# Kernel tuning notes

Measured on AMD Instinct MI355X. Metric: run time of the kernel, lower is better.

Reference implementation:

```python
import jax, jax.numpy as jnp
import numpy as np

N, E, H, IN_FEAT, NUM_GRAPHS, NUM_CLASSES, L, HID = 50000, 600000, 128, 7, 256, 2, 5, 256
EPS_MSG = 1e-7
EPS_SOFTMAX = 1e-16
LN_EPS = 1e-5


def layer_norm(x, g, b):
    mu = jnp.mean(x, axis=-1, keepdims=True)
    var = jnp.mean((x - mu) ** 2, axis=-1, keepdims=True)
    return (x - mu) * jax.lax.rsqrt(var + LN_EPS) * g + b


def setup_inputs() -> dict:
    key = jax.random.key(0)
    ks = jax.random.split(key, 16)
    s = 0.05
    return {
        "x": jax.random.normal(ks[0], (N, IN_FEAT), jnp.float32),
        "edge_index": jax.random.randint(ks[1], (2, E), 0, N),
        "batch": jnp.sort(jax.random.randint(ks[2], (N,), 0, NUM_GRAPHS)),
        "enc_W": jax.random.normal(ks[3], (IN_FEAT, H), jnp.float32) * s,
        "enc_b": jnp.zeros((H,), jnp.float32),
        "t": jnp.ones((L,), jnp.float32),  # learn_t, init t=1.0
        "W1": jax.random.normal(ks[4], (L, H, HID), jnp.float32) * s,
        "b1": jnp.zeros((L, HID), jnp.float32),
        "g1": jnp.ones((L, HID), jnp.float32),
        "bb1": jnp.zeros((L, HID), jnp.float32),
        "W2": jax.random.normal(ks[5], (L, HID, H), jnp.float32) * s,
        "b2": jnp.zeros((L, H), jnp.float32),
        "ln_g": jnp.ones((L, H), jnp.float32),
        "ln_b": jnp.zeros((L, H), jnp.float32),
        "cls_W": jax.random.normal(ks[6], (H, NUM_CLASSES), jnp.float32) * s,
        "cls_b": jnp.zeros((NUM_CLASSES,), jnp.float32),
    }


def reference(x, edge_index, batch, enc_W, enc_b, t, W1, b1, g1, bb1, W2, b2, ln_g, ln_b, cls_W, cls_b):
    n = x.shape[0]
    src, dst = edge_index[0], edge_index[1]  # messages flow src -> dst
    h = x @ enc_W + enc_b  # node_encoder, [N, H]
    for i in range(t.shape[0]):  # DeepGCNLayer, block='res+'
        z = jax.nn.relu(layer_norm(h, ln_g[i], ln_b[i]))
        # GENConv message: relu(x_j) + eps (edge_attr is None)
        msg = jax.nn.relu(z[src]) + EPS_MSG  # [E, H]
        # scatter-softmax aggregation with temperature t
        logits = msg * t[i]
        m = jax.ops.segment_max(logits, dst, num_segments=n)  # [N, H]
        ex = jnp.exp(logits - m[dst])
        den = jax.ops.segment_sum(ex, dst, num_segments=n) + EPS_SOFTMAX
        agg = jax.ops.segment_sum(ex * msg, dst, num_segments=n) / den
        # GENConv update MLP: Linear -> LayerNorm -> ReLU -> Linear on (agg + x)
        out = agg + z
        hm = jax.nn.relu(layer_norm(out @ W1[i] + b1[i], g1[i], bb1[i]))
        h = h + (hm @ W2[i] + b2[i])  # residual
    pooled = jax.ops.segment_sum(h, batch, num_segments=NUM_GRAPHS)  # global_add_pool
    return pooled @ cls_W + cls_b
```

## Files before the change

kernel.cpp:

```cpp
#include <hip/hip_runtime.h>
#include <hip/hip_bf16.h>

#define HD 128
#define HIDD 256
#define EPS_MSG 1e-7f
#define EPS_SM 1e-16f
#define LN_EPS 1e-5f
#define HP2 264
#define LOG2E 1.44269504f

typedef __attribute__((ext_vector_type(8))) short bf16x8;
typedef __attribute__((ext_vector_type(4))) float f32x4;
typedef __attribute__((ext_vector_type(4))) ushort u16x4;

static __device__ __forceinline__ float wave_reduce_sum(float v) {
#pragma unroll
    for (int off = 32; off >= 1; off >>= 1) v += __shfl_xor(v, off, 64);
    return v;
}

static __device__ __forceinline__ float u2f(unsigned v) {
    union { float f; unsigned u; } x;
    x.u = v;
    return x.f;
}
static __device__ __forceinline__ ushort f2bf(float f) {
    __hip_bfloat16 b = __float2bfloat16(f);
    return *(ushort*)&b;
}
static __device__ __forceinline__ unsigned packbf(float lo, float hi) {
    return (unsigned)f2bf(lo) | ((unsigned)f2bf(hi) << 16);
}

__global__ __launch_bounds__(256) void enc_ln_kernel(const float* __restrict__ x,
                                                     const float* __restrict__ W,
                                                     const float* __restrict__ b,
                                                     const float* __restrict__ g,
                                                     const float* __restrict__ bt,
                                                     unsigned* __restrict__ hp,
                                                     unsigned* __restrict__ zp, int N) {
    int node = blockIdx.x * 4 + (threadIdx.x >> 6);
    int lane = threadIdx.x & 63;
    if (node >= N) return;
    float xr[7];
#pragma unroll
    for (int j = 0; j < 7; ++j) xr[j] = x[node * 7 + j];
    float v0 = b[lane], v1 = b[lane + 64];
#pragma unroll
    for (int j = 0; j < 7; ++j) {
        v0 = fmaf(xr[j], W[j * HD + lane], v0);
        v1 = fmaf(xr[j], W[j * HD + lane + 64], v1);
    }
    float s = wave_reduce_sum(v0 + v1);
    float ss = wave_reduce_sum(v0 * v0 + v1 * v1);
    float mu = s * (1.f / 128.f);
    float var = ss * (1.f / 128.f) - mu * mu;
    float rstd = rsqrtf(var + LN_EPS);
    float z0 = fmaxf((v0 - mu) * rstd * g[lane] + bt[lane], 0.f);
    float z1 = fmaxf((v1 - mu) * rstd * g[lane + 64] + bt[lane + 64], 0.f);
    int i0 = (2 * lane) & 63, i1 = (2 * lane + 1) & 63;
    float he_lo = __shfl(v0, i0), ho_lo = __shfl(v0, i1);
    float he_hi = __shfl(v1, i0), ho_hi = __shfl(v1, i1);
    float hce = (lane < 32) ? he_lo : he_hi;
    float hco = (lane < 32) ? ho_lo : ho_hi;
    hp[(size_t)node * 64 + lane] = packbf(hce, hco);
    float e_lo = __shfl(z0, i0), o_lo = __shfl(z0, i1);
    float e_hi = __shfl(z1, i0), o_hi = __shfl(z1, i1);
    float ce = (lane < 32) ? e_lo : e_hi;
    float co = (lane < 32) ? o_lo : o_hi;
    zp[(size_t)node * 64 + lane] = packbf(ce, co);
}

__global__ __launch_bounds__(256) void wconv_kernel(const float* __restrict__ W1,
                                                    const float* __restrict__ W2,
                                                    ushort* __restrict__ W1t,
                                                    ushort* __restrict__ W2t, int L) {
    int gid = blockIdx.x * 256 + threadIdx.x;
    int per = HD * HIDD;
    int tot = L * per;
    if (gid < tot) {
        int l = gid / per, r = gid % per;
        int n = r >> 7, k = r & 127;
        W1t[gid] = f2bf(W1[(size_t)l * per + (size_t)k * HIDD + n]);
    } else if (gid < 2 * tot) {
        int g2 = gid - tot;
        int l = g2 / per, r = g2 % per;
        int n = r >> 8, k = r & 255;
        W2t[g2] = f2bf(W2[(size_t)l * per + (size_t)k * HD + n]);
    }
}

__global__ __launch_bounds__(256) void count_kernel(const int* __restrict__ dst, int* __restrict__ cnt, int E) {
    int e = blockIdx.x * 256 + threadIdx.x;
    if (e < E) atomicAdd(&cnt[dst[e]], 1);
}

__global__ __launch_bounds__(256) void scanA_kernel(const int* __restrict__ cnt, int* __restrict__ row_ptr,
                                                    int* __restrict__ blk_sums, int n) {
    __shared__ int sb[256];
    int tid = threadIdx.x;
    int idx = blockIdx.x * 256 + tid;
    int v = (idx < n) ? cnt[idx] : 0;
    sb[tid] = v;
    __syncthreads();
#pragma unroll
    for (int off = 1; off < 256; off <<= 1) {
        int x = (tid >= off) ? sb[tid - off] : 0;
        __syncthreads();
        sb[tid] += x;
        __syncthreads();
    }
    if (idx < n) row_ptr[idx + 1] = sb[tid];
    if (tid == 255) blk_sums[blockIdx.x] = sb[255];
}

__global__ __launch_bounds__(256) void scanB_kernel(int* __restrict__ blk_sums, int nblk) {
    __shared__ int sb[256];
    int tid = threadIdx.x;
    int v = (tid < nblk) ? blk_sums[tid] : 0;
    sb[tid] = v;
    __syncthreads();
#pragma unroll
    for (int off = 1; off < 256; off <<= 1) {
        int x = (tid >= off) ? sb[tid - off] : 0;
        __syncthreads();
        sb[tid] += x;
        __syncthreads();
    }
    if (tid < nblk) blk_sums[tid] = sb[tid];
}

__global__ __launch_bounds__(256) void scanC_kernel(int* __restrict__ row_ptr, const int* __restrict__ blk_sums, int n) {
    int idx = blockIdx.x * 256 + threadIdx.x;
    if (idx == 0) row_ptr[0] = 0;
    if (idx < n) {
        int b = idx >> 8;
        if (b > 0) row_ptr[idx + 1] += blk_sums[b - 1];
    }
}

__global__ __launch_bounds__(256) void cursor_init_kernel(const int* __restrict__ row_ptr, int* __restrict__ cursor, int n) {
    int idx = blockIdx.x * 256 + threadIdx.x;
    if (idx < n) cursor[idx] = row_ptr[idx];
}

__global__ __launch_bounds__(256) void scatter_kernel(const int* __restrict__ src, const int* __restrict__ dst,
                                                      int* __restrict__ cursor, int* __restrict__ esrc, int E) {
    int e = blockIdx.x * 256 + threadIdx.x;
    if (e < E) {
        int v = dst[e];
        int pos = atomicAdd(&cursor[v], 1);
        esrc[pos] = src[e];
    }
}

__global__ __launch_bounds__(256) void agg_kernel(const unsigned* __restrict__ zp,
                                                  const int* __restrict__ row_ptr,
                                                  const int* __restrict__ esrc,
                                                  const float* __restrict__ t_all, int layer,
                                                  unsigned* __restrict__ obuf, int N) {
    int node = __builtin_amdgcn_readfirstlane(blockIdx.x * 4 + (threadIdx.x >> 6));
    int lane = threadIdx.x & 63;
    if (node >= N) return;
    const float tv = t_all[layer];
    const float M = 12.f * fmaxf(tv, 1.f);
    const float tv2 = tv * LOG2E;
    const float mM2 = -M * LOG2E;
    int beg = row_ptr[node], end = row_ptr[node + 1];

    float se0 = 0.f, se1 = 0.f, sw0 = 0.f, sw1 = 0.f;
    float te0 = 0.f, te1 = 0.f, tw0 = 0.f, tw1 = 0.f;

#define AGG_EDGE(P, E0, E1, W0, W1)                                   \
    {                                                                  \
        float a0 = u2f((P) << 16) + EPS_MSG;                           \
        float a1 = u2f((P) & 0xffff0000u) + EPS_MSG;                   \
        float x0 = __builtin_amdgcn_exp2f(fmaf(a0, tv2, mM2));         \
        float x1 = __builtin_amdgcn_exp2f(fmaf(a1, tv2, mM2));         \
        E0 += x0;                                                      \
        E1 += x1;                                                      \
        W0 = fmaf(x0, a0, W0);                                         \
        W1 = fmaf(x1, a1, W1);                                         \
    }

    int e = beg;
    for (; e + 4 <= end; e += 4) {
        int s0 = esrc[e], s1 = esrc[e + 1], s2 = esrc[e + 2], s3 = esrc[e + 3];
        unsigned p0 = zp[(size_t)s0 * 64 + lane];
        unsigned p1 = zp[(size_t)s1 * 64 + lane];
        unsigned p2 = zp[(size_t)s2 * 64 + lane];
        unsigned p3 = zp[(size_t)s3 * 64 + lane];
        AGG_EDGE(p0, se0, se1, sw0, sw1)
        AGG_EDGE(p1, se0, se1, sw0, sw1)
        AGG_EDGE(p2, te0, te1, tw0, tw1)
        AGG_EDGE(p3, te0, te1, tw0, tw1)
    }
    for (; e < end; ++e) {
        unsigned p0 = zp[(size_t)esrc[e] * 64 + lane];
        AGG_EDGE(p0, se0, se1, sw0, sw1)
    }
#undef AGG_EDGE
    se0 += te0; se1 += te1; sw0 += tw0; sw1 += tw1;

    float a0 = (end > beg) ? sw0 / (se0 + EPS_SM) : 0.f;
    float a1 = (end > beg) ? sw1 / (se1 + EPS_SM) : 0.f;
    unsigned ps = zp[(size_t)node * 64 + lane];
    float z0 = u2f(ps << 16), z1 = u2f(ps & 0xffff0000u);
    obuf[(size_t)node * 64 + lane] = packbf(a0 + z0, a1 + z1);
}

__global__ __launch_bounds__(256, 4) void mlp_kernel(const ushort* __restrict__ obuf,
                                                     unsigned* __restrict__ hp,
                                                     const ushort* __restrict__ W1t, const float* __restrict__ b1,
                                                     const float* __restrict__ g1, const float* __restrict__ bb1,
                                                     const ushort* __restrict__ W2t, const float* __restrict__ b2,
                                                     const float* __restrict__ gnext, const float* __restrict__ btnext,
                                                     unsigned* __restrict__ zp, int fuse,
                                                     int N) {
    __shared__ ushort s_hm[32 * HP2];
    __shared__ float s_part[32 * 8];

    int tid = threadIdx.x;
    int wid = tid >> 6, lane = tid & 63;
    int l15 = lane & 15, q = lane >> 4;
    int row0 = blockIdx.x * 32;

    uint2 hpre[2][2];
#pragma unroll
    for (int mb = 0; mb < 2; ++mb) {
        int row = row0 + mb * 16 + l15;
#pragma unroll
        for (int nb = 0; nb < 2; ++nb) {
            if (row < N)
                hpre[mb][nb] = *(const uint2*)&hp[(size_t)row * 64 + wid * 16 + nb * 8 + q * 2];
            else {
                hpre[mb][nb].x = 0u;
                hpre[mb][nb].y = 0u;
            }
        }
    }

    f32x4 acc1[2][4];
#pragma unroll
    for (int mb = 0; mb < 2; ++mb)
#pragma unroll
        for (int nb = 0; nb < 4; ++nb) acc1[mb][nb] = (f32x4)0.f;

#pragma unroll
    for (int kk = 0; kk < 4; ++kk) {
        bf16x8 bfr[2];
#pragma unroll
        for (int mb = 0; mb < 2; ++mb) {
            int row = row0 + mb * 16 + l15;
            if (row < N)
                bfr[mb] = *(const bf16x8*)(obuf + (size_t)row * HD + kk * 32 + q * 8);
            else
                bfr[mb] = (bf16x8)0;
        }
#pragma unroll
        for (int nb = 0; nb < 4; ++nb) {
            bf16x8 wfr = *(const bf16x8*)&W1t[(size_t)(wid * 64 + nb * 16 + l15) * HD + kk * 32 + q * 8];
#pragma unroll
            for (int mb = 0; mb < 2; ++mb)
                acc1[mb][nb] = __builtin_amdgcn_mfma_f32_16x16x32_bf16(wfr, bfr[mb], acc1[mb][nb], 0, 0, 0);
        }
    }

    f32x4 b1v[4];
#pragma unroll
    for (int nb = 0; nb < 4; ++nb) b1v[nb] = *(const f32x4*)&b1[wid * 64 + nb * 16 + q * 4];

#pragma unroll
    for (int mb = 0; mb < 2; ++mb) {
        float s = 0.f, ss = 0.f;
#pragma unroll
        for (int nb = 0; nb < 4; ++nb) {
#pragma unroll
            for (int rg = 0; rg < 4; ++rg) {
                float v = acc1[mb][nb][rg] + b1v[nb][rg];
                acc1[mb][nb][rg] = v;
                s += v;
                ss += v * v;
            }
        }
        s += __shfl_xor(s, 16, 64);
        s += __shfl_xor(s, 32, 64);
        ss += __shfl_xor(ss, 16, 64);
        ss += __shfl_xor(ss, 32, 64);
        if (q == 0) {
            s_part[(mb * 16 + l15) * 8 + wid * 2] = s;
            s_part[(mb * 16 + l15) * 8 + wid * 2 + 1] = ss;
        }
    }
    __syncthreads();

    f32x4 g1v[4], bbv[4];
#pragma unroll
    for (int nb = 0; nb < 4; ++nb) {
        g1v[nb] = *(const f32x4*)&g1[wid * 64 + nb * 16 + q * 4];
        bbv[nb] = *(const f32x4*)&bb1[wid * 64 + nb * 16 + q * 4];
    }
#pragma unroll
    for (int mb = 0; mb < 2; ++mb) {
        int rl = mb * 16 + l15;
        f32x4 p0 = *(const f32x4*)&s_part[rl * 8];
        f32x4 p1 = *(const f32x4*)&s_part[rl * 8 + 4];
        float S = p0.x + p0.z + p1.x + p1.z;
        float SS = p0.y + p0.w + p1.y + p1.w;
        float mu = S * (1.f / 256.f);
        float var = SS * (1.f / 256.f) - mu * mu;
        float rstd = rsqrtf(var + LN_EPS);
#pragma unroll
        for (int nb = 0; nb < 4; ++nb) {
            u16x4 pk;
#pragma unroll
            for (int rg = 0; rg < 4; ++rg) {
                float v = fmaxf((acc1[mb][nb][rg] - mu) * rstd * g1v[nb][rg] + bbv[nb][rg], 0.f);
                pk[rg] = f2bf(v);
            }
            *(u16x4*)&s_hm[rl * HP2 + wid * 64 + nb * 16 + q * 4] = pk;
        }
    }
    __syncthreads();

    f32x4 acc2[2][2];
#pragma unroll
    for (int mb = 0; mb < 2; ++mb)
#pragma unroll
        for (int nb = 0; nb < 2; ++nb) acc2[mb][nb] = (f32x4)0.f;

#pragma unroll
    for (int kk = 0; kk < 8; ++kk) {
        bf16x8 hfr[2];
#pragma unroll
        for (int mb = 0; mb < 2; ++mb)
            hfr[mb] = *(const bf16x8*)&s_hm[(mb * 16 + l15) * HP2 + kk * 32 + q * 8];
#pragma unroll
        for (int nb = 0; nb < 2; ++nb) {
            bf16x8 wfr = *(const bf16x8*)&W2t[(size_t)(wid * 32 + nb * 16 + l15) * HIDD + kk * 32 + q * 8];
#pragma unroll
            for (int mb = 0; mb < 2; ++mb)
                acc2[mb][nb] = __builtin_amdgcn_mfma_f32_16x16x32_bf16(wfr, hfr[mb], acc2[mb][nb], 0, 0, 0);
        }
    }

    f32x4 b2v[2];
#pragma unroll
    for (int nb = 0; nb < 2; ++nb) b2v[nb] = *(const f32x4*)&b2[wid * 32 + nb * 16 + q * 4];

#pragma unroll
    for (int mb = 0; mb < 2; ++mb) {
        int row = row0 + mb * 16 + l15;
        float s2 = 0.f, ss2 = 0.f;
        if (row < N) {
#pragma unroll
            for (int nb = 0; nb < 2; ++nb) {
                uint2 hv = hpre[mb][nb];
                float h0 = u2f(hv.x << 16), h1 = u2f(hv.x & 0xffff0000u);
                float h2 = u2f(hv.y << 16), h3 = u2f(hv.y & 0xffff0000u);
                f32x4 v;
                v[0] = h0 + acc2[mb][nb][0] + b2v[nb][0];
                v[1] = h1 + acc2[mb][nb][1] + b2v[nb][1];
                v[2] = h2 + acc2[mb][nb][2] + b2v[nb][2];
                v[3] = h3 + acc2[mb][nb][3] + b2v[nb][3];
                s2 += v[0] + v[1] + v[2] + v[3];
                ss2 += v[0] * v[0] + v[1] * v[1] + v[2] * v[2] + v[3] * v[3];
                uint2 pk;
                pk.x = packbf(v[0], v[1]);
                pk.y = packbf(v[2], v[3]);
                *(uint2*)&hp[(size_t)row * 64 + wid * 16 + nb * 8 + q * 2] = pk;
                acc2[mb][nb] = v;
            }
        }
        if (fuse) {
            s2 += __shfl_xor(s2, 16, 64);
            s2 += __shfl_xor(s2, 32, 64);
            ss2 += __shfl_xor(ss2, 16, 64);
            ss2 += __shfl_xor(ss2, 32, 64);
            if (q == 0) {
                s_part[(mb * 16 + l15) * 8 + wid * 2] = s2;
                s_part[(mb * 16 + l15) * 8 + wid * 2 + 1] = ss2;
            }
        }
    }

    if (fuse) {
        __syncthreads();
        f32x4 gnv[2], bnv[2];
#pragma unroll
        for (int nb = 0; nb < 2; ++nb) {
            gnv[nb] = *(const f32x4*)&gnext[wid * 32 + nb * 16 + q * 4];
            bnv[nb] = *(const f32x4*)&btnext[wid * 32 + nb * 16 + q * 4];
        }
#pragma unroll
        for (int mb = 0; mb < 2; ++mb) {
            int rl = mb * 16 + l15;
            int row = row0 + rl;
            f32x4 p0 = *(const f32x4*)&s_part[rl * 8];
            f32x4 p1 = *(const f32x4*)&s_part[rl * 8 + 4];
            float S = p0.x + p0.z + p1.x + p1.z;
            float SS = p0.y + p0.w + p1.y + p1.w;
            float mu = S * (1.f / 128.f);
            float var = SS * (1.f / 128.f) - mu * mu;
            float rstd = rsqrtf(var + LN_EPS);
            if (row < N) {
#pragma unroll
                for (int nb = 0; nb < 2; ++nb) {
                    float z0 = fmaxf((acc2[mb][nb][0] - mu) * rstd * gnv[nb][0] + bnv[nb][0], 0.f);
                    float z1 = fmaxf((acc2[mb][nb][1] - mu) * rstd * gnv[nb][1] + bnv[nb][1], 0.f);
                    float z2 = fmaxf((acc2[mb][nb][2] - mu) * rstd * gnv[nb][2] + bnv[nb][2], 0.f);
                    float z3 = fmaxf((acc2[mb][nb][3] - mu) * rstd * gnv[nb][3] + bnv[nb][3], 0.f);
                    uint2 pk;
                    pk.x = packbf(z0, z1);
                    pk.y = packbf(z2, z3);
                    *(uint2*)&zp[(size_t)row * 64 + wid * 16 + nb * 8 + q * 2] = pk;
                }
            }
        }
    }
}

__global__ __launch_bounds__(256) void pool_kernel(const unsigned* __restrict__ hp,
                                                   const int* __restrict__ batch, int N,
                                                   float* __restrict__ pooled) {
    __shared__ int sb[2];
    __shared__ float red0[256], red1[256];
    int g = blockIdx.x;
    if (threadIdx.x == 0) {
        int lo = 0, hi = N;
        while (lo < hi) { int mid = (lo + hi) >> 1; if (batch[mid] < g) lo = mid + 1; else hi = mid; }
        sb[0] = lo;
        lo = 0; hi = N;
        int gq = g + 1;
        while (lo < hi) { int mid = (lo + hi) >> 1; if (batch[mid] < gq) lo = mid + 1; else hi = mid; }
        sb[1] = lo;
    }
    __syncthreads();
    int beg = sb[0], end = sb[1];
    int c = threadIdx.x & 63, str = threadIdx.x >> 6;
    float a0 = 0.f, a1 = 0.f;
    for (int r = beg + str; r < end; r += 4) {
        unsigned p = hp[(size_t)r * 64 + c];
        a0 += u2f(p << 16);
        a1 += u2f(p & 0xffff0000u);
    }
    red0[threadIdx.x] = a0;
    red1[threadIdx.x] = a1;
    __syncthreads();
    if (str == 0) {
        float s0 = red0[c] + red0[64 + c] + red0[128 + c] + red0[192 + c];
        float s1 = red1[c] + red1[64 + c] + red1[128 + c] + red1[192 + c];
        pooled[(size_t)g * HD + 2 * c] = s0;
        pooled[(size_t)g * HD + 2 * c + 1] = s1;
    }
}

__global__ __launch_bounds__(256) void cls_kernel(const float* __restrict__ pooled,
                                                  const float* __restrict__ W,
                                                  const float* __restrict__ b,
                                                  float* __restrict__ out, int G) {
    int gid = blockIdx.x * 256 + threadIdx.x;
    if (gid >= G * 2) return;
    int g = gid >> 1, cl = gid & 1;
    float acc = b[cl];
#pragma unroll 8
    for (int k = 0; k < HD; ++k) acc += pooled[g * HD + k] * W[k * 2 + cl];
    out[gid] = acc;
}

extern "C" void kernel_launch(void* const* d_in, const int* in_sizes, int n_in,
                              void* d_out, int out_size, void* d_ws, size_t ws_size,
                              hipStream_t stream) {
    const float* x     = (const float*)d_in[0];
    const int*   eidx  = (const int*)d_in[1];
    const int*   batch = (const int*)d_in[2];
    const float* enc_W = (const float*)d_in[3];
    const float* enc_b = (const float*)d_in[4];
    const float* t_all = (const float*)d_in[5];
    const float* W1    = (const float*)d_in[6];
    const float* b1    = (const float*)d_in[7];
    const float* g1    = (const float*)d_in[8];
    const float* bb1   = (const float*)d_in[9];
    const float* W2    = (const float*)d_in[10];
    const float* b2    = (const float*)d_in[11];
    const float* ln_g  = (const float*)d_in[12];
    const float* ln_b  = (const float*)d_in[13];
    const float* cls_W = (const float*)d_in[14];
    const float* cls_b = (const float*)d_in[15];
    float* out = (float*)d_out;

    const int N = in_sizes[0] / 7;
    const int E = in_sizes[1] / 2;
    const int L = in_sizes[5];
    const int G = out_size / 2;
    const int* src = eidx;
    const int* dst = eidx + E;

    char* p = (char*)d_ws;
    auto alloc = [&](size_t bytes) {
        char* q = p;
        p += (bytes + 255) & ~(size_t)255;
        return q;
    };
    unsigned* hp     = (unsigned*)alloc((size_t)N * 64 * 4);
    unsigned* zp     = (unsigned*)alloc((size_t)N * 64 * 4);
    unsigned* obuf   = (unsigned*)alloc((size_t)N * 64 * 4);
    float*    pooled = (float*)alloc((size_t)G * HD * 4);
    int* cnt      = (int*)alloc((size_t)N * 4);
    int* row_ptr  = (int*)alloc((size_t)(N + 1) * 4);
    int* cursor   = (int*)alloc((size_t)N * 4);
    int* blk_sums = (int*)alloc(256 * 4);
    int* esrc     = (int*)alloc((size_t)E * 4);
    ushort* W1t   = (ushort*)alloc((size_t)L * HD * HIDD * 2);
    ushort* W2t   = (ushort*)alloc((size_t)L * HD * HIDD * 2);

    const int nblkN = (N + 255) / 256;
    const int nblkE = (E + 255) / 256;

    enc_ln_kernel<<<(N + 3) / 4, 256, 0, stream>>>(x, enc_W, enc_b, ln_g, ln_b, hp, zp, N);
    {
        int tot2 = 2 * L * HD * HIDD;
        wconv_kernel<<<(tot2 + 255) / 256, 256, 0, stream>>>(W1, W2, W1t, W2t, L);
    }

    hipMemsetAsync(cnt, 0, (size_t)N * 4, stream);
    count_kernel<<<nblkE, 256, 0, stream>>>(dst, cnt, E);
    scanA_kernel<<<nblkN, 256, 0, stream>>>(cnt, row_ptr, blk_sums, N);
    scanB_kernel<<<1, 256, 0, stream>>>(blk_sums, nblkN);
    scanC_kernel<<<nblkN, 256, 0, stream>>>(row_ptr, blk_sums, N);
    cursor_init_kernel<<<nblkN, 256, 0, stream>>>(row_ptr, cursor, N);
    scatter_kernel<<<nblkE, 256, 0, stream>>>(src, dst, cursor, esrc, E);

    for (int i = 0; i < L; ++i) {
        agg_kernel<<<(N + 3) / 4, 256, 0, stream>>>(zp, row_ptr, esrc, t_all, i, obuf, N);
        int fuse = (i + 1 < L) ? 1 : 0;
        const float* gn = ln_g + (size_t)(fuse ? i + 1 : i) * HD;
        const float* bn = ln_b + (size_t)(fuse ? i + 1 : i) * HD;
        mlp_kernel<<<(N + 31) / 32, 256, 0, stream>>>((const ushort*)obuf, hp,
                                                      W1t + (size_t)i * HD * HIDD, b1 + (size_t)i * HIDD,
                                                      g1 + (size_t)i * HIDD, bb1 + (size_t)i * HIDD,
                                                      W2t + (size_t)i * HD * HIDD, b2 + (size_t)i * HD,
                                                      gn, bn, zp, fuse, N);
    }

    pool_kernel<<<G, 256, 0, stream>>>(hp, batch, N, pooled);
    cls_kernel<<<(G * 2 + 255) / 256, 256, 0, stream>>>(pooled, cls_W, cls_b, out, G);
}
```

Baseline: 495.2 us.

## Persistent MLP kernel with register-resident weights, prefetching agg loop, fused cursor init

The MLP kernel becomes persistent with a 512-block grid. Each wave loads its W1 and W2 MFMA fragments into registers once and loops over 32-row tiles, so weights are not re-read per tile; it adds a sync at the top of each tile to protect shared-memory reuse. The aggregation kernel now software-pipelines its gathers, loading the next four source rows before processing the current ones, and issues the self-row load early. The cursor-init kernel is merged into scanC, which removes one launch. Holding the weights in registers raises register pressure (launch bounds occupancy hint dropped), which may cut occupancy.

```diff
diff --git a/kernel.cpp b/kernel.cpp
--- a/kernel.cpp
+++ b/kernel.cpp
@@ -130,18 +130,16 @@
     if (tid < nblk) blk_sums[tid] = sb[tid];
 }
 
-__global__ __launch_bounds__(256) void scanC_kernel(int* __restrict__ row_ptr, const int* __restrict__ blk_sums, int n) {
+__global__ __launch_bounds__(256) void scanC_kernel(int* __restrict__ row_ptr, const int* __restrict__ blk_sums,
+                                                    int* __restrict__ cursor, int n) {
     int idx = blockIdx.x * 256 + threadIdx.x;
-    if (idx == 0) row_ptr[0] = 0;
+    if (idx == 0) { row_ptr[0] = 0; cursor[0] = 0; }
     if (idx < n) {
         int b = idx >> 8;
-        if (b > 0) row_ptr[idx + 1] += blk_sums[b - 1];
-    }
-}
-
-__global__ __launch_bounds__(256) void cursor_init_kernel(const int* __restrict__ row_ptr, int* __restrict__ cursor, int n) {
-    int idx = blockIdx.x * 256 + threadIdx.x;
-    if (idx < n) cursor[idx] = row_ptr[idx];
+        int v = row_ptr[idx + 1] + ((b > 0) ? blk_sums[b - 1] : 0);
+        row_ptr[idx + 1] = v;
+        if (idx + 1 < n) cursor[idx + 1] = v;
+    }
 }
 
 __global__ __launch_bounds__(256) void scatter_kernel(const int* __restrict__ src, const int* __restrict__ dst,
@@ -168,6 +166,8 @@
     const float mM2 = -M * LOG2E;
     int beg = row_ptr[node], end = row_ptr[node + 1];
 
+    unsigned ps = zp[(size_t)node * 64 + lane];
+
     float se0 = 0.f, se1 = 0.f, sw0 = 0.f, sw1 = 0.f;
     float te0 = 0.f, te1 = 0.f, tw0 = 0.f, tw1 = 0.f;
 
@@ -184,16 +184,35 @@
     }
 
     int e = beg;
-    for (; e + 4 <= end; e += 4) {
+    unsigned pc0, pc1, pc2, pc3;
+    int have = 0;
+    if (e + 4 <= end) {
         int s0 = esrc[e], s1 = esrc[e + 1], s2 = esrc[e + 2], s3 = esrc[e + 3];
-        unsigned p0 = zp[(size_t)s0 * 64 + lane];
-        unsigned p1 = zp[(size_t)s1 * 64 + lane];
-        unsigned p2 = zp[(size_t)s2 * 64 + lane];
-        unsigned p3 = zp[(size_t)s3 * 64 + lane];
-        AGG_EDGE(p0, se0, se1, sw0, sw1)
-        AGG_EDGE(p1, se0, se1, sw0, sw1)
-        AGG_EDGE(p2, te0, te1, tw0, tw1)
-        AGG_EDGE(p3, te0, te1, tw0, tw1)
+        pc0 = zp[(size_t)s0 * 64 + lane];
+        pc1 = zp[(size_t)s1 * 64 + lane];
+        pc2 = zp[(size_t)s2 * 64 + lane];
+        pc3 = zp[(size_t)s3 * 64 + lane];
+        have = 4;
+        e += 4;
+    }
+    while (have == 4) {
+        unsigned pn0, pn1, pn2, pn3;
+        int haven = 0;
+        if (e + 4 <= end) {
+            int s0 = esrc[e], s1 = esrc[e + 1], s2 = esrc[e + 2], s3 = esrc[e + 3];
+            pn0 = zp[(size_t)s0 * 64 + lane];
+            pn1 = zp[(size_t)s1 * 64 + lane];
+            pn2 = zp[(size_t)s2 * 64 + lane];
+            pn3 = zp[(size_t)s3 * 64 + lane];
+            haven = 4;
+            e += 4;
+        }
+        AGG_EDGE(pc0, se0, se1, sw0, sw1)
+        AGG_EDGE(pc1, se0, se1, sw0, sw1)
+        AGG_EDGE(pc2, te0, te1, tw0, tw1)
+        AGG_EDGE(pc3, te0, te1, tw0, tw1)
+        pc0 = pn0; pc1 = pn1; pc2 = pn2; pc3 = pn3;
+        have = haven;
     }
     for (; e < end; ++e) {
         unsigned p0 = zp[(size_t)esrc[e] * 64 + lane];
@@ -204,216 +223,220 @@
 
     float a0 = (end > beg) ? sw0 / (se0 + EPS_SM) : 0.f;
     float a1 = (end > beg) ? sw1 / (se1 + EPS_SM) : 0.f;
-    unsigned ps = zp[(size_t)node * 64 + lane];
     float z0 = u2f(ps << 16), z1 = u2f(ps & 0xffff0000u);
     obuf[(size_t)node * 64 + lane] = packbf(a0 + z0, a1 + z1);
 }
 
-__global__ __launch_bounds__(256, 4) void mlp_kernel(const ushort* __restrict__ obuf,
-                                                     unsigned* __restrict__ hp,
-                                                     const ushort* __restrict__ W1t, const float* __restrict__ b1,
-                                                     const float* __restrict__ g1, const float* __restrict__ bb1,
-                                                     const ushort* __restrict__ W2t, const float* __restrict__ b2,
-                                                     const float* __restrict__ gnext, const float* __restrict__ btnext,
-                                                     unsigned* __restrict__ zp, int fuse,
-                                                     int N) {
+__global__ __launch_bounds__(256) void mlp_kernel(const ushort* __restrict__ obuf,
+                                                  unsigned* __restrict__ hp,
+                                                  const ushort* __restrict__ W1t, const float* __restrict__ b1,
+                                                  const float* __restrict__ g1, const float* __restrict__ bb1,
+                                                  const ushort* __restrict__ W2t, const float* __restrict__ b2,
+                                                  const float* __restrict__ gnext, const float* __restrict__ btnext,
+                                                  unsigned* __restrict__ zp, int fuse,
+                                                  int ntiles, int N) {
     __shared__ ushort s_hm[32 * HP2];
     __shared__ float s_part[32 * 8];
 
     int tid = threadIdx.x;
     int wid = tid >> 6, lane = tid & 63;
     int l15 = lane & 15, q = lane >> 4;
-    int row0 = blockIdx.x * 32;
-
-    uint2 hpre[2][2];
-#pragma unroll
-    for (int mb = 0; mb < 2; ++mb) {
-        int row = row0 + mb * 16 + l15;
-#pragma unroll
-        for (int nb = 0; nb < 2; ++nb) {
-            if (row < N)
-                hpre[mb][nb] = *(const uint2*)&hp[(size_t)row * 64 + wid * 16 + nb * 8 + q * 2];
-            else {
-                hpre[mb][nb].x = 0u;
-                hpre[mb][nb].y = 0u;
-            }
-        }
-    }
-
-    f32x4 acc1[2][4];
-#pragma unroll
-    for (int mb = 0; mb < 2; ++mb)
-#pragma unroll
-        for (int nb = 0; nb < 4; ++nb) acc1[mb][nb] = (f32x4)0.f;
-
-#pragma unroll
-    for (int kk = 0; kk < 4; ++kk) {
-        bf16x8 bfr[2];
+
+    bf16x8 w1f[4][4];
+#pragma unroll
+    for (int kk = 0; kk < 4; ++kk)
+#pragma unroll
+        for (int nb = 0; nb < 4; ++nb)
+            w1f[kk][nb] = *(const bf16x8*)&W1t[(size_t)(wid * 64 + nb * 16 + l15) * HD + kk * 32 + q * 8];
+    bf16x8 w2f[8][2];
+#pragma unroll
+    for (int kk = 0; kk < 8; ++kk)
+#pragma unroll
+        for (int nb = 0; nb < 2; ++nb)
+            w2f[kk][nb] = *(const bf16x8*)&W2t[(size_t)(wid * 32 + nb * 16 + l15) * HIDD + kk * 32 + q * 8];
+
+    for (int tile = blockIdx.x; tile < ntiles; tile += gridDim.x) {
+        int row0 = tile * 32;
+
+        uint2 hpre[2][2];
+        bf16x8 bfr[4][2];
 #pragma unroll
         for (int mb = 0; mb < 2; ++mb) {
             int row = row0 + mb * 16 + l15;
-            if (row < N)
-                bfr[mb] = *(const bf16x8*)(obuf + (size_t)row * HD + kk * 32 + q * 8);
-            else
-                bfr[mb] = (bf16x8)0;
-        }
+            if (row < N) {
+#pragma unroll
+                for (int nb = 0; nb < 2; ++nb)
+                    hpre[mb][nb] = *(const uint2*)&hp[(size_t)row * 64 + wid * 16 + nb * 8 + q * 2];
+#pragma unroll
+                for (int kk = 0; kk < 4; ++kk)
+                    bfr[kk][mb] = *(const bf16x8*)(obuf + (size_t)row * HD + kk * 32 + q * 8);
+            } else {
+#pragma unroll
+                for (int nb = 0; nb < 2; ++nb) { hpre[mb][nb].x = 0u; hpre[mb][nb].y = 0u; }
+#pragma unroll
+                for (int kk = 0; kk < 4; ++kk) bfr[kk][mb] = (bf16x8)0;
+            }
+        }
+        __syncthreads();
+
+        f32x4 acc1[2][4];
+#pragma unroll
+        for (int mb = 0; mb < 2; ++mb)
+#pragma unroll
+            for (int nb = 0; nb < 4; ++nb) acc1[mb][nb] = (f32x4)0.f;
+#pragma unroll
+        for (int kk = 0; kk < 4; ++kk)
+#pragma unroll
+            for (int nb = 0; nb < 4; ++nb)
+#pragma unroll
+                for (int mb = 0; mb < 2; ++mb)
+                    acc1[mb][nb] = __builtin_amdgcn_mfma_f32_16x16x32_bf16(w1f[kk][nb], bfr[kk][mb], acc1[mb][nb], 0, 0, 0);
+
+        f32x4 b1v[4];
+#pragma unroll
+        for (int nb = 0; nb < 4; ++nb) b1v[nb] = *(const f32x4*)&b1[wid * 64 + nb * 16 + q * 4];
+#pragma unroll
+        for (int mb = 0; mb < 2; ++mb) {
+            float s = 0.f, ss = 0.f;
+#pragma unroll
+            for (int nb = 0; nb < 4; ++nb) {
+#pragma unroll
+                for (int rg = 0; rg < 4; ++rg) {
+                    float v = acc1[mb][nb][rg] + b1v[nb][rg];
+                    acc1[mb][nb][rg] = v;
+                    s += v;
+                    ss += v * v;
+                }
+            }
+            s += __shfl_xor(s, 16, 64);
+            s += __shfl_xor(s, 32, 64);
+            ss += __shfl_xor(ss, 16, 64);
+            ss += __shfl_xor(ss, 32, 64);
+            if (q == 0) {
+                s_part[(mb * 16 + l15) * 8 + wid * 2] = s;
+                s_part[(mb * 16 + l15) * 8 + wid * 2 + 1] = ss;
+            }
+        }
+        __syncthreads();
+
+        f32x4 g1v[4], bbv[4];
 #pragma unroll
         for (int nb = 0; nb < 4; ++nb) {
-            bf16x8 wfr = *(const bf16x8*)&W1t[(size_t)(wid * 64 + nb * 16 + l15) * HD + kk * 32 + q * 8];
-#pragma unroll
-            for (int mb = 0; mb < 2; ++mb)
-                acc1[mb][nb] = __builtin_amdgcn_mfma_f32_16x16x32_bf16(wfr, bfr[mb], acc1[mb][nb], 0, 0, 0);
-        }
-    }
-
-    f32x4 b1v[4];
-#pragma unroll
-    for (int nb = 0; nb < 4; ++nb) b1v[nb] = *(const f32x4*)&b1[wid * 64 + nb * 16 + q * 4];
-
-#pragma unroll
-    for (int mb = 0; mb < 2; ++mb) {
-        float s = 0.f, ss = 0.f;
-#pragma unroll
-        for (int nb = 0; nb < 4; ++nb) {
-#pragma unroll
-            for (int rg = 0; rg < 4; ++rg) {
-                float v = acc1[mb][nb][rg] + b1v[nb][rg];
-                acc1[mb][nb][rg] = v;
-                s += v;
-                ss += v * v;
-            }
-        }
-        s += __shfl_xor(s, 16, 64);
-        s += __shfl_xor(s, 32, 64);
-        ss += __shfl_xor(ss, 16, 64);
-        ss += __shfl_xor(ss, 32, 64);
-        if (q == 0) {
-            s_part[(mb * 16 + l15) * 8 + wid * 2] = s;
-            s_part[(mb * 16 + l15) * 8 + wid * 2 + 1] = ss;
-        }
-    }
-    __syncthreads();
-
-    f32x4 g1v[4], bbv[4];
-#pragma unroll
-    for (int nb = 0; nb < 4; ++nb) {
-        g1v[nb] = *(const f32x4*)&g1[wid * 64 + nb * 16 + q * 4];
-        bbv[nb] = *(const f32x4*)&bb1[wid * 64 + nb * 16 + q * 4];
-    }
-#pragma unroll
-    for (int mb = 0; mb < 2; ++mb) {
-        int rl = mb * 16 + l15;
-        f32x4 p0 = *(const f32x4*)&s_part[rl * 8];
-        f32x4 p1 = *(const f32x4*)&s_part[rl * 8 + 4];
-        float S = p0.x + p0.z + p1.x + p1.z;
-        float SS = p0.y + p0.w + p1.y + p1.w;
-        float mu = S * (1.f / 256.f);
-        float var = SS * (1.f / 256.f) - mu * mu;
-        float rstd = rsqrtf(var + LN_EPS);
-#pragma unroll
-        for (int nb = 0; nb < 4; ++nb) {
-            u16x4 pk;
-#pragma unroll
-            for (int rg = 0; rg < 4; ++rg) {
-                float v = fmaxf((acc1[mb][nb][rg] - mu) * rstd * g1v[nb][rg] + bbv[nb][rg], 0.f);
-                pk[rg] = f2bf(v);
-            }
-            *(u16x4*)&s_hm[rl * HP2 + wid * 64 + nb * 16 + q * 4] = pk;
-        }
-    }
-    __syncthreads();
-
-    f32x4 acc2[2][2];
-#pragma unroll
-    for (int mb = 0; mb < 2; ++mb)
-#pragma unroll
-        for (int nb = 0; nb < 2; ++nb) acc2[mb][nb] = (f32x4)0.f;
-
-#pragma unroll
-    for (int kk = 0; kk < 8; ++kk) {
-        bf16x8 hfr[2];
-#pragma unroll
-        for (int mb = 0; mb < 2; ++mb)
-            hfr[mb] = *(const bf16x8*)&s_hm[(mb * 16 + l15) * HP2 + kk * 32 + q * 8];
-#pragma unroll
-        for (int nb = 0; nb < 2; ++nb) {
-            bf16x8 wfr = *(const bf16x8*)&W2t[(size_t)(wid * 32 + nb * 16 + l15) * HIDD + kk * 32 + q * 8];
-#pragma unroll
-            for (int mb = 0; mb < 2; ++mb)
-                acc2[mb][nb] = __builtin_amdgcn_mfma_f32_16x16x32_bf16(wfr, hfr[mb], acc2[mb][nb], 0, 0, 0);
-        }
-    }
-
-    f32x4 b2v[2];
-#pragma unroll
-    for (int nb = 0; nb < 2; ++nb) b2v[nb] = *(const f32x4*)&b2[wid * 32 + nb * 16 + q * 4];
-
-#pragma unroll
-    for (int mb = 0; mb < 2; ++mb) {
-        int row = row0 + mb * 16 + l15;
-        float s2 = 0.f, ss2 = 0.f;
-        if (row < N) {
-#pragma unroll
-            for (int nb = 0; nb < 2; ++nb) {
-                uint2 hv = hpre[mb][nb];
-                float h0 = u2f(hv.x << 16), h1 = u2f(hv.x & 0xffff0000u);
-                float h2 = u2f(hv.y << 16), h3 = u2f(hv.y & 0xffff0000u);
-                f32x4 v;
-                v[0] = h0 + acc2[mb][nb][0] + b2v[nb][0];
-                v[1] = h1 + acc2[mb][nb][1] + b2v[nb][1];
-                v[2] = h2 + acc2[mb][nb][2] + b2v[nb][2];
-                v[3] = h3 + acc2[mb][nb][3] + b2v[nb][3];
-                s2 += v[0] + v[1] + v[2] + v[3];
-                ss2 += v[0] * v[0] + v[1] * v[1] + v[2] * v[2] + v[3] * v[3];
-                uint2 pk;
-                pk.x = packbf(v[0], v[1]);
-                pk.y = packbf(v[2], v[3]);
-                *(uint2*)&hp[(size_t)row * 64 + wid * 16 + nb * 8 + q * 2] = pk;
-                acc2[mb][nb] = v;
-            }
-        }
-        if (fuse) {
-            s2 += __shfl_xor(s2, 16, 64);
-            s2 += __shfl_xor(s2, 32, 64);
-            ss2 += __shfl_xor(ss2, 16, 64);
-            ss2 += __shfl_xor(ss2, 32, 64);
-            if (q == 0) {
-                s_part[(mb * 16 + l15) * 8 + wid * 2] = s2;
-                s_part[(mb * 16 + l15) * 8 + wid * 2 + 1] = ss2;
-            }
-        }
-    }
-
-    if (fuse) {
-        __syncthreads();
-        f32x4 gnv[2], bnv[2];
-#pragma unroll
-        for (int nb = 0; nb < 2; ++nb) {
-            gnv[nb] = *(const f32x4*)&gnext[wid * 32 + nb * 16 + q * 4];
-            bnv[nb] = *(const f32x4*)&btnext[wid * 32 + nb * 16 + q * 4];
+            g1v[nb] = *(const f32x4*)&g1[wid * 64 + nb * 16 + q * 4];
+            bbv[nb] = *(const f32x4*)&bb1[wid * 64 + nb * 16 + q * 4];
         }
 #pragma unroll
         for (int mb = 0; mb < 2; ++mb) {
             int rl = mb * 16 + l15;
-            int row = row0 + rl;
             f32x4 p0 = *(const f32x4*)&s_part[rl * 8];
             f32x4 p1 = *(const f32x4*)&s_part[rl * 8 + 4];
             float S = p0.x + p0.z + p1.x + p1.z;
             float SS = p0.y + p0.w + p1.y + p1.w;
-            float mu = S * (1.f / 128.f);
-            float var = SS * (1.f / 128.f) - mu * mu;
+            float mu = S * (1.f / 256.f);
+            float var = SS * (1.f / 256.f) - mu * mu;
             float rstd = rsqrtf(var + LN_EPS);
+#pragma unroll
+            for (int nb = 0; nb < 4; ++nb) {
+                u16x4 pk;
+#pragma unroll
+                for (int rg = 0; rg < 4; ++rg) {
+                    float v = fmaxf((acc1[mb][nb][rg] - mu) * rstd * g1v[nb][rg] + bbv[nb][rg], 0.f);
+                    pk[rg] = f2bf(v);
+                }
+                *(u16x4*)&s_hm[rl * HP2 + wid * 64 + nb * 16 + q * 4] = pk;
+            }
+        }
+        __syncthreads();
+
+        f32x4 acc2[2][2];
+#pragma unroll
+        for (int mb = 0; mb < 2; ++mb)
+#pragma unroll
+            for (int nb = 0; nb < 2; ++nb) acc2[mb][nb] = (f32x4)0.f;
+#pragma unroll
+        for (int kk = 0; kk < 8; ++kk) {
+            bf16x8 hfr[2];
+#pragma unroll
+            for (int mb = 0; mb < 2; ++mb)
+                hfr[mb] = *(const bf16x8*)&s_hm[(mb * 16 + l15) * HP2 + kk * 32 + q * 8];
+#pragma unroll
+            for (int nb = 0; nb < 2; ++nb)
+#pragma unroll
+                for (int mb = 0; mb < 2; ++mb)
+                    acc2[mb][nb] = __builtin_amdgcn_mfma_f32_16x16x32_bf16(w2f[kk][nb], hfr[mb], acc2[mb][nb], 0, 0, 0);
+        }
+
+        f32x4 b2v[2];
+#pragma unroll
+        for (int nb = 0; nb < 2; ++nb) b2v[nb] = *(const f32x4*)&b2[wid * 32 + nb * 16 + q * 4];
+
+#pragma unroll
+        for (int mb = 0; mb < 2; ++mb) {
+            int row = row0 + mb * 16 + l15;
+            float s2 = 0.f, ss2 = 0.f;
             if (row < N) {
 #pragma unroll
                 for (int nb = 0; nb < 2; ++nb) {
-                    float z0 = fmaxf((acc2[mb][nb][0] - mu) * rstd * gnv[nb][0] + bnv[nb][0], 0.f);
-                    float z1 = fmaxf((acc2[mb][nb][1] - mu) * rstd * gnv[nb][1] + bnv[nb][1], 0.f);
-                    float z2 = fmaxf((acc2[mb][nb][2] - mu) * rstd * gnv[nb][2] + bnv[nb][2], 0.f);
-                    float z3 = fmaxf((acc2[mb][nb][3] - mu) * rstd * gnv[nb][3] + bnv[nb][3], 0.f);
+                    uint2 hv = hpre[mb][nb];
+                    float h0 = u2f(hv.x << 16), h1 = u2f(hv.x & 0xffff0000u);
+                    float h2 = u2f(hv.y << 16), h3 = u2f(hv.y & 0xffff0000u);
+                    f32x4 v;
+                    v[0] = h0 + acc2[mb][nb][0] + b2v[nb][0];
+                    v[1] = h1 + acc2[mb][nb][1] + b2v[nb][1];
+                    v[2] = h2 + acc2[mb][nb][2] + b2v[nb][2];
+                    v[3] = h3 + acc2[mb][nb][3] + b2v[nb][3];
+                    s2 += v[0] + v[1] + v[2] + v[3];
+                    ss2 += v[0] * v[0] + v[1] * v[1] + v[2] * v[2] + v[3] * v[3];
                     uint2 pk;
-                    pk.x = packbf(z0, z1);
-                    pk.y = packbf(z2, z3);
-                    *(uint2*)&zp[(size_t)row * 64 + wid * 16 + nb * 8 + q * 2] = pk;
+                    pk.x = packbf(v[0], v[1]);
+                    pk.y = packbf(v[2], v[3]);
+                    *(uint2*)&hp[(size_t)row * 64 + wid * 16 + nb * 8 + q * 2] = pk;
+                    acc2[mb][nb] = v;
+                }
+            }
+            if (fuse) {
+                s2 += __shfl_xor(s2, 16, 64);
+                s2 += __shfl_xor(s2, 32, 64);
+                ss2 += __shfl_xor(ss2, 16, 64);
+                ss2 += __shfl_xor(ss2, 32, 64);
+                if (q == 0) {
+                    s_part[(mb * 16 + l15) * 8 + wid * 2] = s2;
+                    s_part[(mb * 16 + l15) * 8 + wid * 2 + 1] = ss2;
+                }
+            }
+        }
+
+        if (fuse) {
+            __syncthreads();
+            f32x4 gnv[2], bnv[2];
+#pragma unroll
+            for (int nb = 0; nb < 2; ++nb) {
+                gnv[nb] = *(const f32x4*)&gnext[wid * 32 + nb * 16 + q * 4];
+                bnv[nb] = *(const f32x4*)&btnext[wid * 32 + nb * 16 + q * 4];
+            }
+#pragma unroll
+            for (int mb = 0; mb < 2; ++mb) {
+                int rl = mb * 16 + l15;
+                int row = row0 + rl;
+                f32x4 p0 = *(const f32x4*)&s_part[rl * 8];
+                f32x4 p1 = *(const f32x4*)&s_part[rl * 8 + 4];
+                float S = p0.x + p0.z + p1.x + p1.z;
+                float SS = p0.y + p0.w + p1.y + p1.w;
+                float mu = S * (1.f / 128.f);
+                float var = SS * (1.f / 128.f) - mu * mu;
+                float rstd = rsqrtf(var + LN_EPS);
+                if (row < N) {
+#pragma unroll
+                    for (int nb = 0; nb < 2; ++nb) {
+                        float z0 = fmaxf((acc2[mb][nb][0] - mu) * rstd * gnv[nb][0] + bnv[nb][0], 0.f);
+                        float z1 = fmaxf((acc2[mb][nb][1] - mu) * rstd * gnv[nb][1] + bnv[nb][1], 0.f);
+                        float z2 = fmaxf((acc2[mb][nb][2] - mu) * rstd * gnv[nb][2] + bnv[nb][2], 0.f);
+                        float z3 = fmaxf((acc2[mb][nb][3] - mu) * rstd * gnv[nb][3] + bnv[nb][3], 0.f);
+                        uint2 pk;
+                        pk.x = packbf(z0, z1);
+                        pk.y = packbf(z2, z3);
+                        *(uint2*)&zp[(size_t)row * 64 + wid * 16 + nb * 8 + q * 2] = pk;
+                    }
                 }
             }
         }
@@ -516,6 +539,7 @@
 
     const int nblkN = (N + 255) / 256;
     const int nblkE = (E + 255) / 256;
+    const int ntiles = (N + 31) / 32;
 
     enc_ln_kernel<<<(N + 3) / 4, 256, 0, stream>>>(x, enc_W, enc_b, ln_g, ln_b, hp, zp, N);
     {
@@ -527,8 +551,7 @@
     count_kernel<<<nblkE, 256, 0, stream>>>(dst, cnt, E);
     scanA_kernel<<<nblkN, 256, 0, stream>>>(cnt, row_ptr, blk_sums, N);
     scanB_kernel<<<1, 256, 0, stream>>>(blk_sums, nblkN);
-    scanC_kernel<<<nblkN, 256, 0, stream>>>(row_ptr, blk_sums, N);
-    cursor_init_kernel<<<nblkN, 256, 0, stream>>>(row_ptr, cursor, N);
+    scanC_kernel<<<nblkN, 256, 0, stream>>>(row_ptr, blk_sums, cursor, N);
     scatter_kernel<<<nblkE, 256, 0, stream>>>(src, dst, cursor, esrc, E);
 
     for (int i = 0; i < L; ++i) {
@@ -536,11 +559,11 @@
         int fuse = (i + 1 < L) ? 1 : 0;
         const float* gn = ln_g + (size_t)(fuse ? i + 1 : i) * HD;
         const float* bn = ln_b + (size_t)(fuse ? i + 1 : i) * HD;
-        mlp_kernel<<<(N + 31) / 32, 256, 0, stream>>>((const ushort*)obuf, hp,
-                                                      W1t + (size_t)i * HD * HIDD, b1 + (size_t)i * HIDD,
-                                                      g1 + (size_t)i * HIDD, bb1 + (size_t)i * HIDD,
-                                                      W2t + (size_t)i * HD * HIDD, b2 + (size_t)i * HD,
-                                                      gn, bn, zp, fuse, N);
+        mlp_kernel<<<512, 256, 0, stream>>>((const ushort*)obuf, hp,
+                                            W1t + (size_t)i * HD * HIDD, b1 + (size_t)i * HIDD,
+                                            g1 + (size_t)i * HIDD, bb1 + (size_t)i * HIDD,
+                                            W2t + (size_t)i * HD * HIDD, b2 + (size_t)i * HD,
+                                            gn, bn, zp, fuse, ntiles, N);
     }
 
     pool_kernel<<<G, 256, 0, stream>>>(hp, batch, N, pooled);
```

New measurement: 452.1 us. -8.7%, faster.
